# Kernel tuning notes

Hardware: AMD Instinct MI355X
Metric: run time of the kernel (lower is better)

The kernel has to match this reference:

```python
import jax, jax.numpy as jnp
import numpy as np

H = 8          # heads
D = 64         # head_dimension
EMB = 512      # embedding_dimension
B, S, XL, KK = 4, 1024, 1024, 32


def setup_inputs() -> dict:
    key = jax.random.key(0)
    ks = jax.random.split(key, 14)
    HD = H * D
    wsc = EMB ** -0.5
    return {
        "x": jax.random.normal(ks[0], (B, S, EMB), jnp.float32),
        "rel_pos": jax.random.normal(ks[1], (H, S, XL + S), jnp.float32) * 0.02,
        "xl_memory": jax.random.normal(ks[2], (B, XL, 2, HD), jnp.float32),
        "knn_retrieved": jax.random.normal(ks[3], (B, S, KK, 2, HD), jnp.float32),
        "Wq": jax.random.normal(ks[4], (HD, EMB), jnp.float32) * wsc,
        "bq": jnp.zeros((HD,), jnp.float32),
        "Wk": jax.random.normal(ks[5], (HD, EMB), jnp.float32) * wsc,
        "bk": jnp.zeros((HD,), jnp.float32),
        "Wv": jax.random.normal(ks[6], (HD, EMB), jnp.float32) * wsc,
        "bv": jnp.zeros((HD,), jnp.float32),
        "Wo": jax.random.normal(ks[7], (EMB, HD), jnp.float32) * (HD ** -0.5),
        "bo": jnp.zeros((EMB,), jnp.float32),
        "gate": jax.random.normal(ks[8], (H, 1, 1), jnp.float32),
    }


def _split_heads(t):
    # [b, s, h*d] -> [b, h, s, d]
    b, s, _ = t.shape
    return t.reshape(b, s, H, D).transpose(0, 2, 1, 3)


def reference(x, rel_pos, xl_memory, knn_retrieved,
              Wq, bq, Wk, bk, Wv, bv, Wo, bo, gate):
    scale = D ** -0.5
    b, s, _ = x.shape
    xl_len = xl_memory.shape[1]

    q = _split_heads(x @ Wq.T + bq)   # [b,h,s,d]
    k = _split_heads(x @ Wk.T + bk)
    v = _split_heads(x @ Wv.T + bv)

    # XL memory concat (keys/values stacked along dim -2 of xl_memory)
    k_mem = _split_heads(xl_memory[..., 0, :])
    v_mem = _split_heads(xl_memory[..., 1, :])
    k = jnp.concatenate((k_mem, k), axis=2)  # [b,h,j,d], j = xl+s
    v = jnp.concatenate((v_mem, v), axis=2)

    # local causal XL attention; note: rel_pos added BEFORE scaling (as in source)
    qk = jnp.einsum('bhid,bhjd->bhij', q, k)
    i, j = qk.shape[-2:]
    qk = (qk + rel_pos[..., -i:, -j:]) * scale
    mask = jnp.triu(jnp.ones((i, j), dtype=bool), j - i + 1)
    attn = jax.nn.softmax(jnp.where(mask, -jnp.inf, qk), axis=-1)
    qkv = jnp.einsum('bhij,bhjd->bhid', attn, v)

    # kNN external-memory attention over retrieved kv pairs
    kk = knn_retrieved.shape[2]
    k_ext = knn_retrieved[..., 0, :].reshape(b, s, kk, H, D).transpose(0, 3, 1, 2, 4)  # [b,h,s,k,d]
    v_ext = knn_retrieved[..., 1, :].reshape(b, s, kk, H, D).transpose(0, 3, 1, 2, 4)
    qk_ext = jnp.einsum('bhsd,bhskd->bhsk', q, k_ext) * scale
    attn_ext = jax.nn.softmax(qk_ext, axis=-1)
    qkv_ext = jnp.einsum('bhsk,bhskd->bhsd', attn_ext, v_ext)

    g = jax.nn.sigmoid(gate)                # [h,1,1] broadcasts over [b,h,s,d]
    merged = qkv * g + qkv_ext * (1.0 - g)

    out = merged.transpose(0, 2, 1, 3).reshape(b, s, H * D) @ Wo.T + bo

    # current kv memory: flatten heads, stack (k,v), drop the xl prefix
    key_flat = k.transpose(0, 2, 1, 3).reshape(b, j, H * D)
    val_flat = v.transpose(0, 2, 1, 3).reshape(b, j, H * D)
    current_kv_memory = jnp.stack((key_flat, val_flat), axis=-2)[:, xl_len:]

    return out, current_kv_memory
```

## Files before the change

kernel.cpp:

```cpp
#include <hip/hip_runtime.h>
#include <stdint.h>

#define H_ 8
#define D_ 64
#define EMBD 512
#define HD_ 512
#define B_ 4
#define S_ 1024
#define XL_ 1024
#define J_ 2048
#define KK_ 32
#define OUT1 (B_*S_*EMBD)

typedef __bf16 bf16x8 __attribute__((ext_vector_type(8)));
typedef float f32x4 __attribute__((ext_vector_type(4)));

__device__ __forceinline__ uint32_t pack2bf(float a, float b) {
    uint32_t ua = __builtin_bit_cast(uint32_t, a);
    uint32_t ub = __builtin_bit_cast(uint32_t, b);
    ua = (ua + 0x7FFFu + ((ua >> 16) & 1u)) >> 16;
    ub = (ub + 0x7FFFu + ((ub >> 16) & 1u)) >> 16;
    return ua | (ub << 16);
}

#define GPAD 72

__global__ __launch_bounds__(256) void gemm_bt(
    const float* __restrict__ A, const float* __restrict__ W,
    const float* __restrict__ bias, float* __restrict__ out, int mode)
{
    __shared__ uint16_t a_l[64 * GPAD];
    __shared__ uint16_t w_l[64 * GPAD];
    const int t    = threadIdx.x;
    const int m0   = blockIdx.x * 64;
    const int n0   = blockIdx.y * 64;
    const int wv   = t >> 6;
    const int lane = t & 63;
    const int quad = lane >> 4;
    const int l16  = lane & 15;
    const int lrow = t >> 2;
    const int lseg = (t & 3) * 16;

    f32x4 zero = {0.f, 0.f, 0.f, 0.f};
    f32x4 acc[4] = {zero, zero, zero, zero};

    for (int k0 = 0; k0 < EMBD; k0 += 64) {
        const float* ga = A + (size_t)(m0 + lrow) * EMBD + k0 + lseg;
        const float* gw = W + (size_t)(n0 + lrow) * EMBD + k0 + lseg;
        float4 a0 = *(const float4*)(ga);
        float4 a1 = *(const float4*)(ga + 4);
        float4 a2 = *(const float4*)(ga + 8);
        float4 a3 = *(const float4*)(ga + 12);
        float4 w0 = *(const float4*)(gw);
        float4 w1 = *(const float4*)(gw + 4);
        float4 w2 = *(const float4*)(gw + 8);
        float4 w3 = *(const float4*)(gw + 12);
        uint32_t* pa = (uint32_t*)(a_l + lrow * GPAD + lseg);
        uint32_t* pw = (uint32_t*)(w_l + lrow * GPAD + lseg);
        pa[0] = pack2bf(a0.x, a0.y); pa[1] = pack2bf(a0.z, a0.w);
        pa[2] = pack2bf(a1.x, a1.y); pa[3] = pack2bf(a1.z, a1.w);
        pa[4] = pack2bf(a2.x, a2.y); pa[5] = pack2bf(a2.z, a2.w);
        pa[6] = pack2bf(a3.x, a3.y); pa[7] = pack2bf(a3.z, a3.w);
        pw[0] = pack2bf(w0.x, w0.y); pw[1] = pack2bf(w0.z, w0.w);
        pw[2] = pack2bf(w1.x, w1.y); pw[3] = pack2bf(w1.z, w1.w);
        pw[4] = pack2bf(w2.x, w2.y); pw[5] = pack2bf(w2.z, w2.w);
        pw[6] = pack2bf(w3.x, w3.y); pw[7] = pack2bf(w3.z, w3.w);
        __syncthreads();
        #pragma unroll
        for (int ks = 0; ks < 64; ks += 32) {
            bf16x8 af = *(const bf16x8*)(a_l + (wv*16 + l16) * GPAD + ks + quad*8);
            #pragma unroll
            for (int nt = 0; nt < 4; nt++) {
                bf16x8 wf = *(const bf16x8*)(w_l + (nt*16 + l16) * GPAD + ks + quad*8);
                acc[nt] = __builtin_amdgcn_mfma_f32_16x16x32_bf16(af, wf, acc[nt], 0, 0, 0);
            }
        }
        __syncthreads();
    }

    #pragma unroll
    for (int nt = 0; nt < 4; nt++) {
        const int col = n0 + nt*16 + l16;
        const float bvv = bias[col];
        #pragma unroll
        for (int r = 0; r < 4; r++) {
            const int row = m0 + wv*16 + quad*4 + r;
            const float v = acc[nt][r] + bvv;
            if (mode == 0)      out[(size_t)row * EMBD + col] = v;
            else if (mode == 1) out[(size_t)row * 1024 + col] = v;
            else                out[(size_t)row * 1024 + 512 + col] = v;
        }
    }
}

#define APAD 72

__global__ __launch_bounds__(256) void attn_local(
    const float* __restrict__ q_ws,
    const float* __restrict__ xlm,
    const float* __restrict__ kv_cur,
    const float* __restrict__ rel,
    float* __restrict__ o_ws)
{
    __shared__ uint16_t qS[64][APAD];
    __shared__ uint16_t kS[64][APAD];
    __shared__ uint16_t vS[64][APAD];
    __shared__ uint16_t pS[4][16][APAD];

    const int t    = threadIdx.x;
    const int wv   = t >> 6;
    const int lane = t & 63;
    const int quad = lane >> 4;
    const int l16  = lane & 15;
    const int b    = blockIdx.z;
    const int h    = blockIdx.y;
    const int i0   = blockIdx.x * 64;

    {
        const int row = t >> 2;
        const int dc  = (t & 3) * 16;
        const float* g = q_ws + (size_t)(b*S_ + i0 + row) * HD_ + h*D_ + dc;
        float4 x0 = *(const float4*)(g);
        float4 x1 = *(const float4*)(g + 4);
        float4 x2 = *(const float4*)(g + 8);
        float4 x3 = *(const float4*)(g + 12);
        uint32_t* d = (uint32_t*)&qS[row][dc];
        d[0] = pack2bf(x0.x, x0.y); d[1] = pack2bf(x0.z, x0.w);
        d[2] = pack2bf(x1.x, x1.y); d[3] = pack2bf(x1.z, x1.w);
        d[4] = pack2bf(x2.x, x2.y); d[5] = pack2bf(x2.z, x2.w);
        d[6] = pack2bf(x3.x, x3.y); d[7] = pack2bf(x3.z, x3.w);
    }

    f32x4 zero = {0.f, 0.f, 0.f, 0.f};
    f32x4 accO[4] = {zero, zero, zero, zero};
    float m_r[4], l_r[4];
    #pragma unroll
    for (int r = 0; r < 4; r++) { m_r[r] = -1e30f; l_r[r] = 0.f; }

    const int irow0  = i0 + wv*16 + quad*4;
    const int ntiles = ((i0 + XL_ + 63) >> 6) + 1;
    const float scale = 0.125f;

    const int kj  = t >> 2;
    const int kdc = (t & 3) * 16;
    const int vj  = (t & 31) * 2;
    const int vdc = (t >> 5) * 8;

    for (int tix = 0; tix < ntiles; tix++) {
        const int j0 = tix << 6;
        {
            const int jg = j0 + kj;
            const float* g = (jg < XL_)
                ? xlm    + ((size_t)(b*XL_ + jg) * 2    ) * HD_ + h*D_ + kdc
                : kv_cur + ((size_t)(b*S_ + (jg - XL_)) * 2) * HD_ + h*D_ + kdc;
            float4 x0 = *(const float4*)(g);
            float4 x1 = *(const float4*)(g + 4);
            float4 x2 = *(const float4*)(g + 8);
            float4 x3 = *(const float4*)(g + 12);
            uint32_t* d = (uint32_t*)&kS[kj][kdc];
            d[0] = pack2bf(x0.x, x0.y); d[1] = pack2bf(x0.z, x0.w);
            d[2] = pack2bf(x1.x, x1.y); d[3] = pack2bf(x1.z, x1.w);
            d[4] = pack2bf(x2.x, x2.y); d[5] = pack2bf(x2.z, x2.w);
            d[6] = pack2bf(x3.x, x3.y); d[7] = pack2bf(x3.z, x3.w);
        }
        {
            const int jg = j0 + vj;
            const float* g0 = (jg < XL_)
                ? xlm    + ((size_t)(b*XL_ + jg) * 2 + 1) * HD_ + h*D_ + vdc
                : kv_cur + ((size_t)(b*S_ + (jg - XL_)) * 2 + 1) * HD_ + h*D_ + vdc;
            const float* g1 = g0 + 2*HD_;
            float4 a0 = *(const float4*)(g0);
            float4 a1 = *(const float4*)(g0 + 4);
            float4 b0 = *(const float4*)(g1);
            float4 b1 = *(const float4*)(g1 + 4);
            *(uint32_t*)&vS[vdc+0][vj] = pack2bf(a0.x, b0.x);
            *(uint32_t*)&vS[vdc+1][vj] = pack2bf(a0.y, b0.y);
            *(uint32_t*)&vS[vdc+2][vj] = pack2bf(a0.z, b0.z);
            *(uint32_t*)&vS[vdc+3][vj] = pack2bf(a0.w, b0.w);
            *(uint32_t*)&vS[vdc+4][vj] = pack2bf(a1.x, b1.x);
            *(uint32_t*)&vS[vdc+5][vj] = pack2bf(a1.y, b1.y);
            *(uint32_t*)&vS[vdc+6][vj] = pack2bf(a1.z, b1.z);
            *(uint32_t*)&vS[vdc+7][vj] = pack2bf(a1.w, b1.w);
        }
        __syncthreads();

        float srel[4][4];
        const float* relbase = rel + ((size_t)h*S_ + irow0) * J_ + j0 + l16;
        #pragma unroll
        for (int r = 0; r < 4; r++)
            #pragma unroll
            for (int jt = 0; jt < 4; jt++)
                srel[r][jt] = relbase[(size_t)r * J_ + jt*16];

        bf16x8 aq0 = *(const bf16x8*)&qS[wv*16 + l16][quad*8];
        bf16x8 aq1 = *(const bf16x8*)&qS[wv*16 + l16][32 + quad*8];
        f32x4 sac[4] = {zero, zero, zero, zero};
        #pragma unroll
        for (int jt = 0; jt < 4; jt++) {
            bf16x8 bk0 = *(const bf16x8*)&kS[jt*16 + l16][quad*8];
            bf16x8 bk1 = *(const bf16x8*)&kS[jt*16 + l16][32 + quad*8];
            sac[jt] = __builtin_amdgcn_mfma_f32_16x16x32_bf16(aq0, bk0, sac[jt], 0, 0, 0);
            sac[jt] = __builtin_amdgcn_mfma_f32_16x16x32_bf16(aq1, bk1, sac[jt], 0, 0, 0);
        }

        const bool need_mask = (j0 + 64 > i0 + XL_);

        float p_[4][4];
        float alpha[4];
        #pragma unroll
        for (int r = 0; r < 4; r++) {
            const int irow = irow0 + r;
            float sv[4];
            #pragma unroll
            for (int jt = 0; jt < 4; jt++) {
                float s = (sac[jt][r] + srel[r][jt]) * scale;
                if (need_mask && (j0 + jt*16 + l16 > irow + XL_)) s = -1e30f;
                sv[jt] = s;
            }
            float mx = fmaxf(fmaxf(sv[0], sv[1]), fmaxf(sv[2], sv[3]));
            #pragma unroll
            for (int off = 8; off >= 1; off >>= 1)
                mx = fmaxf(mx, __shfl_xor(mx, off));
            const float mnew = fmaxf(m_r[r], mx);
            alpha[r] = __expf(m_r[r] - mnew);
            m_r[r] = mnew;
            float ps = 0.f;
            #pragma unroll
            for (int jt = 0; jt < 4; jt++) {
                p_[jt][r] = __expf(sv[jt] - mnew);
                ps += p_[jt][r];
            }
            #pragma unroll
            for (int off = 8; off >= 1; off >>= 1)
                ps += __shfl_xor(ps, off);
            l_r[r] = l_r[r] * alpha[r] + ps;
        }
        #pragma unroll
        for (int dt = 0; dt < 4; dt++)
            #pragma unroll
            for (int r = 0; r < 4; r++)
                accO[dt][r] *= alpha[r];

        #pragma unroll
        for (int jt = 0; jt < 4; jt++)
            #pragma unroll
            for (int r = 0; r < 4; r++)
                pS[wv][quad*4 + r][jt*16 + l16] = (uint16_t)pack2bf(p_[jt][r], 0.f);

        #pragma unroll
        for (int kc = 0; kc < 2; kc++) {
            bf16x8 ap = *(const bf16x8*)&pS[wv][l16][kc*32 + quad*8];
            #pragma unroll
            for (int dt = 0; dt < 4; dt++) {
                bf16x8 bv = *(const bf16x8*)&vS[dt*16 + l16][kc*32 + quad*8];
                accO[dt] = __builtin_amdgcn_mfma_f32_16x16x32_bf16(ap, bv, accO[dt], 0, 0, 0);
            }
        }
        __syncthreads();
    }

    #pragma unroll
    for (int r = 0; r < 4; r++) {
        const float inv = 1.f / l_r[r];
        float* o = o_ws + (size_t)(b*S_ + irow0 + r) * HD_ + h*D_ + l16;
        #pragma unroll
        for (int dt = 0; dt < 4; dt++)
            o[dt*16] = accO[dt][r] * inv;
    }
}

__global__ __launch_bounds__(512) void knn_merge(
    const float* __restrict__ q_ws, const float* __restrict__ knn,
    const float* __restrict__ o_ws, const float* __restrict__ gate,
    float* __restrict__ merged)
{
    __shared__ float p_s[H_][KK_];
    const int t    = threadIdx.x;
    const int wv   = t >> 6;
    const int lane = t & 63;
    const size_t bs = blockIdx.x;
    const float* base = knn + bs * (size_t)(KK_ * 2 * HD_);
    const float qv = q_ws[bs * HD_ + t];

    #pragma unroll 4
    for (int kk = 0; kk < KK_; kk++) {
        float pr = qv * base[(size_t)(kk*2) * HD_ + t];
        #pragma unroll
        for (int off = 32; off >= 1; off >>= 1)
            pr += __shfl_xor(pr, off);
        if (lane == 0) p_s[wv][kk] = pr;
    }
    __syncthreads();

    const float sval = p_s[wv][lane & 31] * 0.125f;
    float mx = sval;
    #pragma unroll
    for (int off = 16; off >= 1; off >>= 1)
        mx = fmaxf(mx, __shfl_xor(mx, off));
    const float e = __expf(sval - mx);
    float es = e;
    #pragma unroll
    for (int off = 16; off >= 1; off >>= 1)
        es += __shfl_xor(es, off);
    if (lane < 32) p_s[wv][lane] = e / es;
    __syncthreads();

    float acc = 0.f;
    #pragma unroll 4
    for (int kk = 0; kk < KK_; kk++)
        acc += p_s[wv][kk] * base[(size_t)(kk*2 + 1) * HD_ + t];

    const float g = 1.f / (1.f + __expf(-gate[wv]));
    const float o = o_ws[bs * HD_ + t];
    merged[bs * HD_ + t] = o * g + acc * (1.f - g);
}

extern "C" void kernel_launch(void* const* d_in, const int* in_sizes, int n_in,
                              void* d_out, int out_size, void* d_ws, size_t ws_size,
                              hipStream_t stream)
{
    (void)in_sizes; (void)n_in; (void)out_size; (void)ws_size;
    const float* x    = (const float*)d_in[0];
    const float* rel  = (const float*)d_in[1];
    const float* xlm  = (const float*)d_in[2];
    const float* knn  = (const float*)d_in[3];
    const float* Wq   = (const float*)d_in[4];
    const float* bq   = (const float*)d_in[5];
    const float* Wk   = (const float*)d_in[6];
    const float* bk   = (const float*)d_in[7];
    const float* Wv   = (const float*)d_in[8];
    const float* bv   = (const float*)d_in[9];
    const float* Wo   = (const float*)d_in[10];
    const float* bo   = (const float*)d_in[11];
    const float* gate = (const float*)d_in[12];

    float* out    = (float*)d_out;
    float* kv_out = out + OUT1;
    float* q_ws   = (float*)d_ws;
    float* o_ws   = q_ws + OUT1;
    float* mg_ws  = o_ws + OUT1;

    dim3 gg(64, 8, 1);
    gemm_bt<<<gg, 256, 0, stream>>>(x, Wq, bq, q_ws, 0);
    gemm_bt<<<gg, 256, 0, stream>>>(x, Wk, bk, kv_out, 1);
    gemm_bt<<<gg, 256, 0, stream>>>(x, Wv, bv, kv_out, 2);
    attn_local<<<dim3(16, 8, 4), 256, 0, stream>>>(q_ws, xlm, kv_out, rel, o_ws);
    knn_merge<<<dim3(4096), 512, 0, stream>>>(q_ws, knn, o_ws, gate, mg_ws);
    gemm_bt<<<gg, 256, 0, stream>>>(mg_ws, Wo, bo, out, 0);
}
```

Before: 974.0 us.

## Prefetch next K/V and GEMM tiles into registers and fuse QKV launches

Register-prefetches the next k-slice of A/W in the GEMM and the next K/V tile in the local attention loop, so global loads overlap MFMA and softmax work instead of stalling before each tile. The three Q/K/V projection launches are merged into one grid with a z dimension selecting the weight, bias and output. The Q fragment loads are hoisted out of the attention loop. This raises register pressure, which may lower occupancy.

```diff
diff --git a/kernel.cpp b/kernel.cpp
--- a/kernel.cpp
+++ b/kernel.cpp
@@ -25,15 +25,12 @@
 
 #define GPAD 72
 
-__global__ __launch_bounds__(256) void gemm_bt(
+__device__ __forceinline__ void gemm_tile_body(
     const float* __restrict__ A, const float* __restrict__ W,
-    const float* __restrict__ bias, float* __restrict__ out, int mode)
-{
-    __shared__ uint16_t a_l[64 * GPAD];
-    __shared__ uint16_t w_l[64 * GPAD];
+    const float* __restrict__ bias, float* __restrict__ out, int mode,
+    uint16_t* a_l, uint16_t* w_l, int m0, int n0)
+{
     const int t    = threadIdx.x;
-    const int m0   = blockIdx.x * 64;
-    const int n0   = blockIdx.y * 64;
     const int wv   = t >> 6;
     const int lane = t & 63;
     const int quad = lane >> 4;
@@ -41,20 +38,22 @@
     const int lrow = t >> 2;
     const int lseg = (t & 3) * 16;
 
+    const float* gab = A + (size_t)(m0 + lrow) * EMBD + lseg;
+    const float* gwb = W + (size_t)(n0 + lrow) * EMBD + lseg;
+
     f32x4 zero = {0.f, 0.f, 0.f, 0.f};
     f32x4 acc[4] = {zero, zero, zero, zero};
 
+    float4 a0 = *(const float4*)(gab);
+    float4 a1 = *(const float4*)(gab + 4);
+    float4 a2 = *(const float4*)(gab + 8);
+    float4 a3 = *(const float4*)(gab + 12);
+    float4 w0 = *(const float4*)(gwb);
+    float4 w1 = *(const float4*)(gwb + 4);
+    float4 w2 = *(const float4*)(gwb + 8);
+    float4 w3 = *(const float4*)(gwb + 12);
+
     for (int k0 = 0; k0 < EMBD; k0 += 64) {
-        const float* ga = A + (size_t)(m0 + lrow) * EMBD + k0 + lseg;
-        const float* gw = W + (size_t)(n0 + lrow) * EMBD + k0 + lseg;
-        float4 a0 = *(const float4*)(ga);
-        float4 a1 = *(const float4*)(ga + 4);
-        float4 a2 = *(const float4*)(ga + 8);
-        float4 a3 = *(const float4*)(ga + 12);
-        float4 w0 = *(const float4*)(gw);
-        float4 w1 = *(const float4*)(gw + 4);
-        float4 w2 = *(const float4*)(gw + 8);
-        float4 w3 = *(const float4*)(gw + 12);
         uint32_t* pa = (uint32_t*)(a_l + lrow * GPAD + lseg);
         uint32_t* pw = (uint32_t*)(w_l + lrow * GPAD + lseg);
         pa[0] = pack2bf(a0.x, a0.y); pa[1] = pack2bf(a0.z, a0.w);
@@ -66,6 +65,20 @@
         pw[4] = pack2bf(w2.x, w2.y); pw[5] = pack2bf(w2.z, w2.w);
         pw[6] = pack2bf(w3.x, w3.y); pw[7] = pack2bf(w3.z, w3.w);
         __syncthreads();
+
+        if (k0 + 64 < EMBD) {
+            const float* ga = gab + k0 + 64;
+            const float* gw = gwb + k0 + 64;
+            a0 = *(const float4*)(ga);
+            a1 = *(const float4*)(ga + 4);
+            a2 = *(const float4*)(ga + 8);
+            a3 = *(const float4*)(ga + 12);
+            w0 = *(const float4*)(gw);
+            w1 = *(const float4*)(gw + 4);
+            w2 = *(const float4*)(gw + 8);
+            w3 = *(const float4*)(gw + 12);
+        }
+
         #pragma unroll
         for (int ks = 0; ks < 64; ks += 32) {
             bf16x8 af = *(const bf16x8*)(a_l + (wv*16 + l16) * GPAD + ks + quad*8);
@@ -91,6 +104,31 @@
             else                out[(size_t)row * 1024 + 512 + col] = v;
         }
     }
+}
+
+__global__ __launch_bounds__(256) void gemm_bt(
+    const float* __restrict__ A, const float* __restrict__ W,
+    const float* __restrict__ bias, float* __restrict__ out, int mode)
+{
+    __shared__ uint16_t a_l[64 * GPAD];
+    __shared__ uint16_t w_l[64 * GPAD];
+    gemm_tile_body(A, W, bias, out, mode, a_l, w_l, blockIdx.x * 64, blockIdx.y * 64);
+}
+
+__global__ __launch_bounds__(256) void gemm_qkv(
+    const float* __restrict__ A,
+    const float* __restrict__ Wq, const float* __restrict__ bq,
+    const float* __restrict__ Wk, const float* __restrict__ bk,
+    const float* __restrict__ Wv, const float* __restrict__ bv,
+    float* __restrict__ q_ws, float* __restrict__ kv_out)
+{
+    __shared__ uint16_t a_l[64 * GPAD];
+    __shared__ uint16_t w_l[64 * GPAD];
+    const int mode = blockIdx.z;
+    const float* W    = (mode == 0) ? Wq : (mode == 1) ? Wk : Wv;
+    const float* bias = (mode == 0) ? bq : (mode == 1) ? bk : bv;
+    float* out        = (mode == 0) ? q_ws : kv_out;
+    gemm_tile_body(A, W, bias, out, mode, a_l, w_l, blockIdx.x * 64, blockIdx.y * 64);
 }
 
 #define APAD 72
@@ -115,6 +153,15 @@
     const int b    = blockIdx.z;
     const int h    = blockIdx.y;
     const int i0   = blockIdx.x * 64;
+
+    const int irow0  = i0 + wv*16 + quad*4;
+    const int ntiles = ((i0 + XL_ + 63) >> 6) + 1;
+    const float scale = 0.125f;
+
+    const int kj  = t >> 2;
+    const int kdc = (t & 3) * 16;
+    const int vj  = (t & 31) * 2;
+    const int vdc = (t >> 5) * 8;
 
     {
         const int row = t >> 2;
@@ -131,69 +178,86 @@
         d[6] = pack2bf(x3.x, x3.y); d[7] = pack2bf(x3.z, x3.w);
     }
 
+    float4 kx0, kx1, kx2, kx3, va0, va1, vb0, vb1;
+    {
+        const int jg = kj;
+        const float* g = (jg < XL_)
+            ? xlm + ((size_t)(b*XL_ + jg) * 2) * HD_ + h*D_ + kdc
+            : kv_cur + ((size_t)(b*S_ + (jg - XL_)) * 2) * HD_ + h*D_ + kdc;
+        kx0 = *(const float4*)(g);
+        kx1 = *(const float4*)(g + 4);
+        kx2 = *(const float4*)(g + 8);
+        kx3 = *(const float4*)(g + 12);
+        const int jgv = vj;
+        const float* g0 = (jgv < XL_)
+            ? xlm + ((size_t)(b*XL_ + jgv) * 2 + 1) * HD_ + h*D_ + vdc
+            : kv_cur + ((size_t)(b*S_ + (jgv - XL_)) * 2 + 1) * HD_ + h*D_ + vdc;
+        va0 = *(const float4*)(g0);
+        va1 = *(const float4*)(g0 + 4);
+        vb0 = *(const float4*)(g0 + 2*HD_);
+        vb1 = *(const float4*)(g0 + 2*HD_ + 4);
+    }
+
+    __syncthreads();
+    const bf16x8 aq0 = *(const bf16x8*)&qS[wv*16 + l16][quad*8];
+    const bf16x8 aq1 = *(const bf16x8*)&qS[wv*16 + l16][32 + quad*8];
+
     f32x4 zero = {0.f, 0.f, 0.f, 0.f};
     f32x4 accO[4] = {zero, zero, zero, zero};
     float m_r[4], l_r[4];
     #pragma unroll
     for (int r = 0; r < 4; r++) { m_r[r] = -1e30f; l_r[r] = 0.f; }
 
-    const int irow0  = i0 + wv*16 + quad*4;
-    const int ntiles = ((i0 + XL_ + 63) >> 6) + 1;
-    const float scale = 0.125f;
-
-    const int kj  = t >> 2;
-    const int kdc = (t & 3) * 16;
-    const int vj  = (t & 31) * 2;
-    const int vdc = (t >> 5) * 8;
+    const float* relbase = rel + ((size_t)h*S_ + irow0) * J_ + l16;
 
     for (int tix = 0; tix < ntiles; tix++) {
         const int j0 = tix << 6;
         {
-            const int jg = j0 + kj;
+            uint32_t* d = (uint32_t*)&kS[kj][kdc];
+            d[0] = pack2bf(kx0.x, kx0.y); d[1] = pack2bf(kx0.z, kx0.w);
+            d[2] = pack2bf(kx1.x, kx1.y); d[3] = pack2bf(kx1.z, kx1.w);
+            d[4] = pack2bf(kx2.x, kx2.y); d[5] = pack2bf(kx2.z, kx2.w);
+            d[6] = pack2bf(kx3.x, kx3.y); d[7] = pack2bf(kx3.z, kx3.w);
+        }
+        {
+            *(uint32_t*)&vS[vdc+0][vj] = pack2bf(va0.x, vb0.x);
+            *(uint32_t*)&vS[vdc+1][vj] = pack2bf(va0.y, vb0.y);
+            *(uint32_t*)&vS[vdc+2][vj] = pack2bf(va0.z, vb0.z);
+            *(uint32_t*)&vS[vdc+3][vj] = pack2bf(va0.w, vb0.w);
+            *(uint32_t*)&vS[vdc+4][vj] = pack2bf(va1.x, vb1.x);
+            *(uint32_t*)&vS[vdc+5][vj] = pack2bf(va1.y, vb1.y);
+            *(uint32_t*)&vS[vdc+6][vj] = pack2bf(va1.z, vb1.z);
+            *(uint32_t*)&vS[vdc+7][vj] = pack2bf(va1.w, vb1.w);
+        }
+        __syncthreads();
+
+        if (tix + 1 < ntiles) {
+            const int jg = j0 + 64 + kj;
             const float* g = (jg < XL_)
-                ? xlm    + ((size_t)(b*XL_ + jg) * 2    ) * HD_ + h*D_ + kdc
+                ? xlm + ((size_t)(b*XL_ + jg) * 2) * HD_ + h*D_ + kdc
                 : kv_cur + ((size_t)(b*S_ + (jg - XL_)) * 2) * HD_ + h*D_ + kdc;
-            float4 x0 = *(const float4*)(g);
-            float4 x1 = *(const float4*)(g + 4);
-            float4 x2 = *(const float4*)(g + 8);
-            float4 x3 = *(const float4*)(g + 12);
-            uint32_t* d = (uint32_t*)&kS[kj][kdc];
-            d[0] = pack2bf(x0.x, x0.y); d[1] = pack2bf(x0.z, x0.w);
-            d[2] = pack2bf(x1.x, x1.y); d[3] = pack2bf(x1.z, x1.w);
-            d[4] = pack2bf(x2.x, x2.y); d[5] = pack2bf(x2.z, x2.w);
-            d[6] = pack2bf(x3.x, x3.y); d[7] = pack2bf(x3.z, x3.w);
-        }
-        {
-            const int jg = j0 + vj;
-            const float* g0 = (jg < XL_)
-                ? xlm    + ((size_t)(b*XL_ + jg) * 2 + 1) * HD_ + h*D_ + vdc
-                : kv_cur + ((size_t)(b*S_ + (jg - XL_)) * 2 + 1) * HD_ + h*D_ + vdc;
-            const float* g1 = g0 + 2*HD_;
-            float4 a0 = *(const float4*)(g0);
-            float4 a1 = *(const float4*)(g0 + 4);
-            float4 b0 = *(const float4*)(g1);
-            float4 b1 = *(const float4*)(g1 + 4);
-            *(uint32_t*)&vS[vdc+0][vj] = pack2bf(a0.x, b0.x);
-            *(uint32_t*)&vS[vdc+1][vj] = pack2bf(a0.y, b0.y);
-            *(uint32_t*)&vS[vdc+2][vj] = pack2bf(a0.z, b0.z);
-            *(uint32_t*)&vS[vdc+3][vj] = pack2bf(a0.w, b0.w);
-            *(uint32_t*)&vS[vdc+4][vj] = pack2bf(a1.x, b1.x);
-            *(uint32_t*)&vS[vdc+5][vj] = pack2bf(a1.y, b1.y);
-            *(uint32_t*)&vS[vdc+6][vj] = pack2bf(a1.z, b1.z);
-            *(uint32_t*)&vS[vdc+7][vj] = pack2bf(a1.w, b1.w);
-        }
-        __syncthreads();
+            kx0 = *(const float4*)(g);
+            kx1 = *(const float4*)(g + 4);
+            kx2 = *(const float4*)(g + 8);
+            kx3 = *(const float4*)(g + 12);
+            const int jgv = j0 + 64 + vj;
+            const float* g0 = (jgv < XL_)
+                ? xlm + ((size_t)(b*XL_ + jgv) * 2 + 1) * HD_ + h*D_ + vdc
+                : kv_cur + ((size_t)(b*S_ + (jgv - XL_)) * 2 + 1) * HD_ + h*D_ + vdc;
+            va0 = *(const float4*)(g0);
+            va1 = *(const float4*)(g0 + 4);
+            vb0 = *(const float4*)(g0 + 2*HD_);
+            vb1 = *(const float4*)(g0 + 2*HD_ + 4);
+        }
 
         float srel[4][4];
-        const float* relbase = rel + ((size_t)h*S_ + irow0) * J_ + j0 + l16;
+        const float* rb = relbase + j0;
         #pragma unroll
         for (int r = 0; r < 4; r++)
             #pragma unroll
             for (int jt = 0; jt < 4; jt++)
-                srel[r][jt] = relbase[(size_t)r * J_ + jt*16];
-
-        bf16x8 aq0 = *(const bf16x8*)&qS[wv*16 + l16][quad*8];
-        bf16x8 aq1 = *(const bf16x8*)&qS[wv*16 + l16][32 + quad*8];
+                srel[r][jt] = rb[(size_t)r * J_ + jt*16];
+
         f32x4 sac[4] = {zero, zero, zero, zero};
         #pragma unroll
         for (int jt = 0; jt < 4; jt++) {
@@ -340,11 +404,8 @@
     float* o_ws   = q_ws + OUT1;
     float* mg_ws  = o_ws + OUT1;
 
-    dim3 gg(64, 8, 1);
-    gemm_bt<<<gg, 256, 0, stream>>>(x, Wq, bq, q_ws, 0);
-    gemm_bt<<<gg, 256, 0, stream>>>(x, Wk, bk, kv_out, 1);
-    gemm_bt<<<gg, 256, 0, stream>>>(x, Wv, bv, kv_out, 2);
+    gemm_qkv<<<dim3(64, 8, 3), 256, 0, stream>>>(x, Wq, bq, Wk, bk, Wv, bv, q_ws, kv_out);
     attn_local<<<dim3(16, 8, 4), 256, 0, stream>>>(q_ws, xlm, kv_out, rel, o_ws);
     knn_merge<<<dim3(4096), 512, 0, stream>>>(q_ws, knn, o_ws, gate, mg_ws);
-    gemm_bt<<<gg, 256, 0, stream>>>(mg_ws, Wo, bo, out, 0);
-}
+    gemm_bt<<<dim3(64, 8, 1), 256, 0, stream>>>(mg_ws, Wo, bo, out, 0);
+}
```

New measurement: 934.6 us. 1.04x faster.
